# Performance work log

Hardware: AMD Instinct MI355X
Metric: run time of the kernel (lower is better)

## Reference

```python
import jax, jax.numpy as jnp
import numpy as np

# Grid config (LSS standard, matches init_kwargs)
XB = (-50.0, 50.0, 0.5)
YB = (-50.0, 50.0, 0.5)
ZB = (-10.0, 10.0, 20.0)
DB = (4.0, 45.0, 1.0)
FINAL_DIM = (256, 704)
DOWN = 16
CAMC = 64

DX = jnp.array([XB[2], YB[2], ZB[2]], jnp.float32)
BX = jnp.array([XB[0] + XB[2] / 2.0, YB[0] + YB[2] / 2.0, ZB[0] + ZB[2] / 2.0], jnp.float32)
NX0 = int((XB[1] - XB[0]) / XB[2])  # 200
NX1 = int((YB[1] - YB[0]) / YB[2])  # 200
NZ = int((ZB[1] - ZB[0]) / ZB[2])   # 1


def make_frustum():
    ogfH, ogfW = FINAL_DIM
    fH, fW = ogfH // DOWN, ogfW // DOWN
    ds = jnp.arange(DB[0], DB[1], DB[2], dtype=jnp.float32)  # [D]
    D = ds.shape[0]
    ds = jnp.broadcast_to(ds[:, None, None], (D, fH, fW))
    xs = jnp.broadcast_to(jnp.linspace(0.0, ogfW - 1, fW, dtype=jnp.float32)[None, None, :], (D, fH, fW))
    ys = jnp.broadcast_to(jnp.linspace(0.0, ogfH - 1, fH, dtype=jnp.float32)[None, :, None], (D, fH, fW))
    return jnp.stack((xs, ys, ds), -1)  # [D, fH, fW, 3]


def setup_inputs() -> dict:
    key = jax.random.key(0)
    B, N, D, fH, fW, C = 4, 6, 41, 16, 44, CAMC
    kx, kt = jax.random.split(key, 2)
    x = jax.random.normal(kx, (B, N, D, fH, fW, C), jnp.float32)
    # cam-to-ego base: cam z(forward)->ego x, cam x(right)->-ego y, cam y(down)->-ego z
    base = np.array([[0.0, 0.0, 1.0], [-1.0, 0.0, 0.0], [0.0, -1.0, 0.0]], np.float32)
    yaws = np.linspace(0.0, 2.0 * np.pi, N, endpoint=False).astype(np.float32)
    c, s = np.cos(yaws), np.sin(yaws)
    Rz = np.zeros((N, 3, 3), np.float32)
    Rz[:, 0, 0] = c; Rz[:, 0, 1] = -s; Rz[:, 1, 0] = s; Rz[:, 1, 1] = c; Rz[:, 2, 2] = 1.0
    rots_np = np.einsum('nij,jk->nik', Rz, base)
    rots = jnp.asarray(np.tile(rots_np[None], (B, 1, 1, 1)))
    # pinhole intrinsics for 704x256 image
    K = np.array([[550.0, 0.0, 352.0], [0.0, 550.0, 128.0], [0.0, 0.0, 1.0]], np.float32)
    intrins = jnp.asarray(np.tile(K[None, None], (B, N, 1, 1)))
    post_rots = jnp.asarray(np.tile(np.eye(3, dtype=np.float32)[None, None], (B, N, 1, 1)))
    post_trans = jnp.zeros((B, N, 3), jnp.float32)
    trans = jax.random.uniform(kt, (B, N, 3), jnp.float32, -1.5, 1.5)
    return {"x": x, "rots": rots, "trans": trans, "intrins": intrins,
            "post_rots": post_rots, "post_trans": post_trans}


def _forward(x, rots, trans, intrins, post_rots, post_trans):
    B, N, D, fH, fW, C = x.shape
    frustum = make_frustum()  # [D,fH,fW,3]

    # ---- get_geometry ----
    intrins_inv = jnp.linalg.inv(intrins)        # [B,N,3,3]
    post_rots_inv = jnp.linalg.inv(post_rots)    # [B,N,3,3]
    cam_to_ego = rots @ intrins_inv              # [B,N,3,3]
    pts = frustum[None, None] - post_trans[:, :, None, None, None, :]        # [B,N,D,fH,fW,3]
    # points @ post_rots_inv^T  ==  post_rots_inv @ points
    pts = jnp.einsum('bndhwc,bnkc->bndhwk', pts, post_rots_inv)
    pts = jnp.concatenate([pts[..., :2] * pts[..., 2:3], pts[..., 2:3]], -1)
    geom = jnp.einsum('bndhwc,bnkc->bndhwk', pts, cam_to_ego) + trans[:, :, None, None, None, :]

    # ---- voxel_pooling ----
    Nprime = B * N * D * fH * fW
    feats = x.reshape(Nprime, C)
    g = (geom - (BX - DX / 2.0)) / DX
    g = jnp.clip(g, -1e6, 1e6)
    g = jnp.trunc(g).astype(jnp.int32).reshape(Nprime, 3)  # torch .long() truncates toward zero
    batch_ix = jnp.repeat(jnp.arange(B, dtype=jnp.int32), Nprime // B)
    kept = ((g[:, 0] >= 0) & (g[:, 0] < NX0) &
            (g[:, 1] >= 0) & (g[:, 1] < NX1) &
            (g[:, 2] >= 0) & (g[:, 2] < NZ))
    # flat index into [B, NZ, NX0, NX1]; sort+cumsum_trick+scatter == segment-sum per voxel
    idx = batch_ix * (NZ * NX0 * NX1) + g[:, 2] * (NX0 * NX1) + g[:, 0] * NX1 + g[:, 1]
    idx = jnp.where(kept, idx, 0)
    w = kept.astype(feats.dtype)[:, None]
    pooled = jax.ops.segment_sum(feats * w, idx, num_segments=B * NZ * NX0 * NX1)
    final = pooled.reshape(B, NZ, NX0, NX1, C)
    # torch.cat(final.unbind(dim=2), 1) on [B,C,NZ,X,Y] -> [B, NZ*C, X, Y] (z-major)
    final = jnp.transpose(final, (0, 1, 4, 2, 3)).reshape(B, NZ * C, NX0, NX1)
    return final


def reference(x, rots, trans, intrins, post_rots, post_trans):
    return _forward(x, rots, trans, intrins, post_rots, post_trans)
```

## Files before the change

kernel.cpp:

```cpp
#include <hip/hip_runtime.h>
#include <cstddef>

#define NB   4
#define NN_  6
#define ND_  41
#define NFH  16
#define NFW  44
#define NC   64
#define NX0_ 200
#define NX1_ 200
#define NXY  (NX0_ * NX1_)
#define NCOL (NB * NN_ * ND_ * NFW)
#define NCELL (NB * NXY)
#define CAP   48
#define QMAX  (64 * CAP)

__device__ __forceinline__ void inv3(const float* a, float* inv) {
    float c00 = __fsub_rn(__fmul_rn(a[4], a[8]), __fmul_rn(a[5], a[7]));
    float c01 = __fsub_rn(__fmul_rn(a[5], a[6]), __fmul_rn(a[3], a[8]));
    float c02 = __fsub_rn(__fmul_rn(a[3], a[7]), __fmul_rn(a[4], a[6]));
    float det = __fadd_rn(__fadd_rn(__fmul_rn(a[0], c00), __fmul_rn(a[1], c01)),
                          __fmul_rn(a[2], c02));
    inv[0] = __fdiv_rn(c00, det);
    inv[1] = __fdiv_rn(__fsub_rn(__fmul_rn(a[2], a[7]), __fmul_rn(a[1], a[8])), det);
    inv[2] = __fdiv_rn(__fsub_rn(__fmul_rn(a[1], a[5]), __fmul_rn(a[2], a[4])), det);
    inv[3] = __fdiv_rn(c01, det);
    inv[4] = __fdiv_rn(__fsub_rn(__fmul_rn(a[0], a[8]), __fmul_rn(a[2], a[6])), det);
    inv[5] = __fdiv_rn(__fsub_rn(__fmul_rn(a[2], a[3]), __fmul_rn(a[0], a[5])), det);
    inv[6] = __fdiv_rn(c02, det);
    inv[7] = __fdiv_rn(__fsub_rn(__fmul_rn(a[1], a[6]), __fmul_rn(a[0], a[7])), det);
    inv[8] = __fdiv_rn(__fsub_rn(__fmul_rn(a[0], a[4]), __fmul_rn(a[1], a[3])), det);
}

__global__ void setup_kernel(const float* __restrict__ rots,
                             const float* __restrict__ trans,
                             const float* __restrict__ intrins,
                             const float* __restrict__ post_rots,
                             const float* __restrict__ post_trans,
                             float* __restrict__ mats) {
    int t = threadIdx.x;
    if (t >= NB * NN_) return;
    const float* R  = rots      + t * 9;
    const float* K  = intrins   + t * 9;
    const float* PR = post_rots + t * 9;
    float Kinv[9], Pinv[9];
    inv3(K, Kinv);
    inv3(PR, Pinv);
    float* o = mats + t * 24;
    for (int i = 0; i < 3; ++i)
        for (int k = 0; k < 3; ++k) {
            float s = __fmul_rn(R[i * 3 + 0], Kinv[0 * 3 + k]);
            s = __fadd_rn(s, __fmul_rn(R[i * 3 + 1], Kinv[1 * 3 + k]));
            s = __fadd_rn(s, __fmul_rn(R[i * 3 + 2], Kinv[2 * 3 + k]));
            o[i * 3 + k] = s;
        }
    for (int i = 0; i < 9; ++i) o[9 + i] = Pinv[i];
    o[18] = trans[t * 3 + 0];
    o[19] = trans[t * 3 + 1];
    o[20] = trans[t * 3 + 2];
    o[21] = post_trans[t * 3 + 0];
    o[22] = post_trans[t * 3 + 1];
    o[23] = post_trans[t * 3 + 2];
}

__device__ __forceinline__ void hw_fadd(float* p, float v) {
    asm volatile("global_atomic_add_f32 %0, %1, off" : : "v"(p), "v"(v) : "memory");
}

__device__ __forceinline__ int compute_idx(int b, int n, int d, int h, int w,
                                           const float* __restrict__ mats) {
    const float* mp = mats + (b * NN_ + n) * 24;

    float u   = (w == NFW - 1) ? 703.0f : (float)((double)w * (703.0 / 43.0));
    float v   = __fmul_rn((float)h, 17.0f);
    float dep = (float)(4 + d);

    float f0 = __fsub_rn(u, mp[21]);
    float f1 = __fsub_rn(v, mp[22]);
    float f2 = __fsub_rn(dep, mp[23]);

    float q0 = __fadd_rn(__fadd_rn(__fmul_rn(mp[9],  f0), __fmul_rn(mp[10], f1)), __fmul_rn(mp[11], f2));
    float q1 = __fadd_rn(__fadd_rn(__fmul_rn(mp[12], f0), __fmul_rn(mp[13], f1)), __fmul_rn(mp[14], f2));
    float q2 = __fadd_rn(__fadd_rn(__fmul_rn(mp[15], f0), __fmul_rn(mp[16], f1)), __fmul_rn(mp[17], f2));

    float r0 = __fmul_rn(q0, q2);
    float r1 = __fmul_rn(q1, q2);

    float g0 = __fadd_rn(__fadd_rn(__fadd_rn(__fmul_rn(mp[0], r0), __fmul_rn(mp[1], r1)), __fmul_rn(mp[2], q2)), mp[18]);
    float g1 = __fadd_rn(__fadd_rn(__fadd_rn(__fmul_rn(mp[3], r0), __fmul_rn(mp[4], r1)), __fmul_rn(mp[5], q2)), mp[19]);
    float g2 = __fadd_rn(__fadd_rn(__fadd_rn(__fmul_rn(mp[6], r0), __fmul_rn(mp[7], r1)), __fmul_rn(mp[8], q2)), mp[20]);

    float s0 = __fdiv_rn(__fsub_rn(g0, -50.0f), 0.5f);
    float s1 = __fdiv_rn(__fsub_rn(g1, -50.0f), 0.5f);
    float s2 = __fdiv_rn(__fsub_rn(g2, -10.0f), 20.0f);
    s0 = fminf(fmaxf(s0, -1e6f), 1e6f);
    s1 = fminf(fmaxf(s1, -1e6f), 1e6f);
    s2 = fminf(fmaxf(s2, -1e6f), 1e6f);
    int i0 = (int)s0;
    int i1 = (int)s1;
    int i2 = (int)s2;
    if (i0 >= 0 && i0 < NX0_ && i1 >= 0 && i1 < NX1_ && i2 >= 0 && i2 < 1)
        return b * NXY + i0 * NX1_ + i1;
    return -1;
}

__global__ __launch_bounds__(256) void build_lists(const float* __restrict__ mats,
                                                   int* __restrict__ cnt,
                                                   unsigned* __restrict__ lists) {
    int cid = blockIdx.x * 256 + threadIdx.x;
    if (cid >= NCOL) return;
    int w = cid % NFW; int t = cid / NFW;
    int d = t % ND_;   t /= ND_;
    int n = t % NN_;   int b = t / NN_;

    int first = -1;
    unsigned vm = 0, sm = 0;
    #pragma unroll
    for (int h = 0; h < 16; ++h) {
        int ih = compute_idx(b, n, d, h, w, mats);
        bool val = (ih >= 0);
        vm |= (val ? 1u : 0u) << h;
        if (first < 0 && val) first = ih;
        sm |= ((val && ih == first) ? 1u : 0u) << h;
    }
    if (vm == 0) return;
    if (sm == vm) {
        int slot = atomicAdd(&cnt[first], 1);
        if (slot < CAP) lists[(size_t)first * CAP + slot] = (vm << 16) | (unsigned)(cid & 0xffff);
    } else {
        #pragma unroll
        for (int h = 0; h < 16; ++h) {
            int ih = compute_idx(b, n, d, h, w, mats);
            if (ih >= 0) {
                int slot = atomicAdd(&cnt[ih], 1);
                if (slot < CAP) lists[(size_t)ih * CAP + slot] = (1u << (16 + h)) | (unsigned)(cid & 0xffff);
            }
        }
    }
}

__global__ __launch_bounds__(256) void gather_bev(const float* __restrict__ x,
                                                  const int* __restrict__ cnt,
                                                  const unsigned* __restrict__ lists,
                                                  float* __restrict__ out) {
    __shared__ float4 tile[64 * 16];
    __shared__ unsigned short items[QMAX];
    __shared__ int qcount;

    int b   = blockIdx.y;
    int xy0 = blockIdx.x * 64;

    if (threadIdx.x == 0) qcount = 0;
    #pragma unroll
    for (int s = 0; s < 4; ++s)
        tile[s * 256 + threadIdx.x] = make_float4(0.f, 0.f, 0.f, 0.f);
    __syncthreads();

    if (threadIdx.x < 64) {
        int ci = threadIdx.x;
        int c  = cnt[b * NXY + xy0 + ci];
        c = c < CAP ? c : CAP;
        if (c > 0) {
            int base = atomicAdd(&qcount, c);
            for (int e = 0; e < c; ++e)
                items[base + e] = (unsigned short)((ci << 8) | e);
        }
    }
    __syncthreads();
    int total = qcount;

    int g = threadIdx.x >> 4;
    int l = threadIdx.x & 15;
    const int HS = NFW * (NC / 4);

    for (int i = g; i < total; i += 16) {
        unsigned it = items[i];
        int ci = it >> 8, e = it & 255;
        unsigned ent = lists[(size_t)(b * NXY + xy0 + ci) * CAP + e];
        int cid = ent & 0xffff;
        unsigned hmask = ent >> 16;
        int w = cid % NFW; int t2 = cid / NFW;
        int d = t2 % ND_;  t2 /= ND_;
        int n = t2 % NN_;
        const float4* xp = (const float4*)
            (x + (((size_t)((b * NN_ + n) * ND_ + d) * NFH) * NFW + w) * NC) + l;

        float4 a = make_float4(0.f, 0.f, 0.f, 0.f);
        float4 v[8];
        #pragma unroll
        for (int j = 0; j < 8; ++j) v[j] = xp[j * HS];
        #pragma unroll
        for (int j = 0; j < 8; ++j) {
            float m = ((hmask >> j) & 1) ? 1.0f : 0.0f;
            a.x += v[j].x * m; a.y += v[j].y * m;
            a.z += v[j].z * m; a.w += v[j].w * m;
        }
        #pragma unroll
        for (int j = 0; j < 8; ++j) v[j] = xp[(8 + j) * HS];
        #pragma unroll
        for (int j = 0; j < 8; ++j) {
            float m = ((hmask >> (8 + j)) & 1) ? 1.0f : 0.0f;
            a.x += v[j].x * m; a.y += v[j].y * m;
            a.z += v[j].z * m; a.w += v[j].w * m;
        }

        float* tp = (float*)&tile[ci * 16 + (l ^ ((ci >> 2) & 15))];
        atomicAdd(tp + 0, a.x);
        atomicAdd(tp + 1, a.y);
        atomicAdd(tp + 2, a.z);
        atomicAdd(tp + 3, a.w);
    }
    __syncthreads();

    int lane = threadIdx.x & 63, wv = threadIdx.x >> 6;
    int q = lane & 15, lh = lane >> 4, i0 = q << 2;
    #pragma unroll
    for (int s = 0; s < 4; ++s) {
        int c  = s * 16 + wv * 4 + lh;
        int c4 = c >> 2, cr = c & 3;
        float4 vv;
        vv.x = ((const float*)&tile[(i0 + 0) * 16 + (c4 ^ q)])[cr];
        vv.y = ((const float*)&tile[(i0 + 1) * 16 + (c4 ^ q)])[cr];
        vv.z = ((const float*)&tile[(i0 + 2) * 16 + (c4 ^ q)])[cr];
        vv.w = ((const float*)&tile[(i0 + 3) * 16 + (c4 ^ q)])[cr];
        *(float4*)(out + ((size_t)(b * NC + c)) * NXY + xy0 + i0) = vv;
    }
}

__global__ __launch_bounds__(256) void col_pool_direct(const float* __restrict__ x,
                                                       const float* __restrict__ mats,
                                                       float* __restrict__ dst) {
    int cid = blockIdx.x * 8 + (threadIdx.x >> 5);
    int sub = threadIdx.x & 31;
    int l   = sub & 15;
    int hh  = sub >> 4;
    int w = cid % NFW; int t = cid / NFW;
    int d = t % ND_;   t /= ND_;
    int n = t % NN_;   int b = t / NN_;

    int myidx = compute_idx(b, n, d, l, w, mats);
    int idx8[8];
    #pragma unroll
    for (int j = 0; j < 8; ++j) idx8[j] = __shfl(myidx, hh * 8 + j, 32);

    int vmax = myidx;
    #pragma unroll
    for (int k = 1; k < 16; k <<= 1) vmax = max(vmax, __shfl_xor(vmax, k, 16));
    if (vmax < 0) return;

    const float4* xp = (const float4*)
        (x + (((size_t)((b * NN_ + n) * ND_ + d) * NFH) * NFW + w) * NC) + l;
    const int HSTRIDE = NFW * (NC / 4);
    #pragma unroll
    for (int j = 0; j < 8; ++j) {
        if (idx8[j] >= 0) {
            float4 v = xp[(hh * 8 + j) * HSTRIDE];
            int bb = idx8[j] / NXY, xy = idx8[j] % NXY;
            float* o = dst + ((size_t)(bb * NC + l * 4)) * NXY + xy;
            hw_fadd(o,           v.x);
            hw_fadd(o + NXY,     v.y);
            hw_fadd(o + 2 * NXY, v.z);
            hw_fadd(o + 3 * NXY, v.w);
        }
    }
}

extern "C" void kernel_launch(void* const* d_in, const int* in_sizes, int n_in,
                              void* d_out, int out_size, void* d_ws, size_t ws_size,
                              hipStream_t stream) {
    (void)in_sizes; (void)n_in; (void)out_size;
    const float* x          = (const float*)d_in[0];
    const float* rots       = (const float*)d_in[1];
    const float* trans      = (const float*)d_in[2];
    const float* intrins    = (const float*)d_in[3];
    const float* post_rots  = (const float*)d_in[4];
    const float* post_trans = (const float*)d_in[5];
    float* out = (float*)d_out;

    const size_t need = ((size_t)NCELL * (CAP + 1) + 1024) * sizeof(int);

    if (ws_size >= need) {
        int*      cnt   = (int*)d_ws;
        unsigned* lists = (unsigned*)(cnt + NCELL);
        float*    mats  = (float*)(lists + (size_t)NCELL * CAP);
        setup_kernel<<<1, 32, 0, stream>>>(rots, trans, intrins, post_rots, post_trans, mats);
        hipMemsetAsync(cnt, 0, (size_t)NCELL * sizeof(int), stream);
        build_lists<<<(NCOL + 255) / 256, 256, 0, stream>>>(mats, cnt, lists);
        gather_bev<<<dim3(NXY / 64, NB), 256, 0, stream>>>(x, cnt, lists, out);
    } else {
        float* mats = (float*)d_ws;
        setup_kernel<<<1, 32, 0, stream>>>(rots, trans, intrins, post_rots, post_trans, mats);
        hipMemsetAsync(out, 0, (size_t)NB * NC * NXY * sizeof(float), stream);
        col_pool_direct<<<NCOL / 8, 256, 0, stream>>>(x, mats, out);
    }
}
```

Measured before the change: 293.0 us.

## Precompute per-column feature sums while building voxel lists, gather sums in BEV pass

The list-building kernel now uses 16 threads per column. Each thread computes one height's voxel index, and shuffle reductions find the column's valid mask and whether all valid heights land in the same voxel. The same kernel streams x once in order and writes a masked per-column channel sum to a workspace buffer. The gather kernel then reads a single precomputed 256-byte sum when the list entry covers the full column, instead of 16 strided float4 loads per entry. It falls back to per-height loads only for split columns. The trade is an extra write and read of the colsum buffer and a larger workspace requirement, in exchange for streaming x sequentially rather than through scattered gather loads.

```diff
diff --git a/kernel.cpp b/kernel.cpp
--- a/kernel.cpp
+++ b/kernel.cpp
@@ -104,44 +104,91 @@
     return -1;
 }
 
-__global__ __launch_bounds__(256) void build_lists(const float* __restrict__ mats,
-                                                   int* __restrict__ cnt,
-                                                   unsigned* __restrict__ lists) {
-    int cid = blockIdx.x * 256 + threadIdx.x;
-    if (cid >= NCOL) return;
+__global__ __launch_bounds__(256) void colsum_build(const float* __restrict__ x,
+                                                    const float* __restrict__ mats,
+                                                    int* __restrict__ cnt,
+                                                    unsigned* __restrict__ lists,
+                                                    unsigned* __restrict__ aux,
+                                                    float4* __restrict__ colsum) {
+    int cid = blockIdx.x * 16 + (threadIdx.x >> 4);
+    int l   = threadIdx.x & 15;
     int w = cid % NFW; int t = cid / NFW;
     int d = t % ND_;   t /= ND_;
     int n = t % NN_;   int b = t / NN_;
 
-    int first = -1;
-    unsigned vm = 0, sm = 0;
-    #pragma unroll
-    for (int h = 0; h < 16; ++h) {
-        int ih = compute_idx(b, n, d, h, w, mats);
-        bool val = (ih >= 0);
-        vm |= (val ? 1u : 0u) << h;
-        if (first < 0 && val) first = ih;
-        sm |= ((val && ih == first) ? 1u : 0u) << h;
-    }
-    if (vm == 0) return;
-    if (sm == vm) {
-        int slot = atomicAdd(&cnt[first], 1);
-        if (slot < CAP) lists[(size_t)first * CAP + slot] = (vm << 16) | (unsigned)(cid & 0xffff);
+    int myidx = compute_idx(b, n, d, l, w, mats);
+
+    int vm   = (myidx >= 0) ? (1 << l) : 0;
+    int vmin = (myidx >= 0) ? myidx : 0x7fffffff;
+    int vmax = myidx;
+    #pragma unroll
+    for (int k = 1; k < 16; k <<= 1) {
+        vm  |= __shfl_xor(vm,  k, 16);
+        vmin = min(vmin, __shfl_xor(vmin, k, 16));
+        vmax = max(vmax, __shfl_xor(vmax, k, 16));
+    }
+    if (vmax < 0) return;
+    bool allsame = (vmin == vmax);
+
+    if (allsame) {
+        if (l == 0) {
+            int slot = atomicAdd(&cnt[vmax], 1);
+            if (slot < CAP)
+                lists[(size_t)vmax * CAP + slot] = ((unsigned)vm << 16) | (unsigned)cid;
+        }
     } else {
-        #pragma unroll
-        for (int h = 0; h < 16; ++h) {
-            int ih = compute_idx(b, n, d, h, w, mats);
-            if (ih >= 0) {
-                int slot = atomicAdd(&cnt[ih], 1);
-                if (slot < CAP) lists[(size_t)ih * CAP + slot] = (1u << (16 + h)) | (unsigned)(cid & 0xffff);
-            }
-        }
-    }
+        if (myidx >= 0) {
+            int slot = atomicAdd(&cnt[myidx], 1);
+            if (slot < CAP)
+                lists[(size_t)myidx * CAP + slot] = (1u << (16 + l)) | (unsigned)cid;
+        }
+    }
+    if (l == 0) aux[cid] = (unsigned)vm;
+
+    const float4* xp = (const float4*)
+        (x + (((size_t)((b * NN_ + n) * ND_ + d) * NFH) * NFW + w) * NC) + l;
+    const int HS = NFW * (NC / 4);
+
+    float4 v[8];
+    float4 A0 = make_float4(0.f, 0.f, 0.f, 0.f);
+    float4 A1 = make_float4(0.f, 0.f, 0.f, 0.f);
+    #pragma unroll
+    for (int j = 0; j < 8; ++j) v[j] = xp[j * HS];
+    #pragma unroll
+    for (int j = 0; j < 8; j += 2) {
+        float m0 = ((vm >> j) & 1) ? 1.0f : 0.0f;
+        float m1 = ((vm >> (j + 1)) & 1) ? 1.0f : 0.0f;
+        A0.x += v[j].x * m0;     A0.y += v[j].y * m0;
+        A0.z += v[j].z * m0;     A0.w += v[j].w * m0;
+        A1.x += v[j + 1].x * m1; A1.y += v[j + 1].y * m1;
+        A1.z += v[j + 1].z * m1; A1.w += v[j + 1].w * m1;
+    }
+    float4 s0 = make_float4(A0.x + A1.x, A0.y + A1.y, A0.z + A1.z, A0.w + A1.w);
+
+    float4 B0 = make_float4(0.f, 0.f, 0.f, 0.f);
+    float4 B1 = make_float4(0.f, 0.f, 0.f, 0.f);
+    #pragma unroll
+    for (int j = 0; j < 8; ++j) v[j] = xp[(8 + j) * HS];
+    #pragma unroll
+    for (int j = 0; j < 8; j += 2) {
+        float m0 = ((vm >> (8 + j)) & 1) ? 1.0f : 0.0f;
+        float m1 = ((vm >> (9 + j)) & 1) ? 1.0f : 0.0f;
+        B0.x += v[j].x * m0;     B0.y += v[j].y * m0;
+        B0.z += v[j].z * m0;     B0.w += v[j].w * m0;
+        B1.x += v[j + 1].x * m1; B1.y += v[j + 1].y * m1;
+        B1.z += v[j + 1].z * m1; B1.w += v[j + 1].w * m1;
+    }
+    float4 s1 = make_float4(B0.x + B1.x, B0.y + B1.y, B0.z + B1.z, B0.w + B1.w);
+
+    colsum[(size_t)cid * 16 + l] =
+        make_float4(s0.x + s1.x, s0.y + s1.y, s0.z + s1.z, s0.w + s1.w);
 }
 
 __global__ __launch_bounds__(256) void gather_bev(const float* __restrict__ x,
                                                   const int* __restrict__ cnt,
                                                   const unsigned* __restrict__ lists,
+                                                  const unsigned* __restrict__ aux,
+                                                  const float4* __restrict__ colsum,
                                                   float* __restrict__ out) {
     __shared__ float4 tile[64 * 16];
     __shared__ unsigned short items[QMAX];
@@ -179,29 +226,24 @@
         unsigned ent = lists[(size_t)(b * NXY + xy0 + ci) * CAP + e];
         int cid = ent & 0xffff;
         unsigned hmask = ent >> 16;
-        int w = cid % NFW; int t2 = cid / NFW;
-        int d = t2 % ND_;  t2 /= ND_;
-        int n = t2 % NN_;
-        const float4* xp = (const float4*)
-            (x + (((size_t)((b * NN_ + n) * ND_ + d) * NFH) * NFW + w) * NC) + l;
-
-        float4 a = make_float4(0.f, 0.f, 0.f, 0.f);
-        float4 v[8];
-        #pragma unroll
-        for (int j = 0; j < 8; ++j) v[j] = xp[j * HS];
-        #pragma unroll
-        for (int j = 0; j < 8; ++j) {
-            float m = ((hmask >> j) & 1) ? 1.0f : 0.0f;
-            a.x += v[j].x * m; a.y += v[j].y * m;
-            a.z += v[j].z * m; a.w += v[j].w * m;
-        }
-        #pragma unroll
-        for (int j = 0; j < 8; ++j) v[j] = xp[(8 + j) * HS];
-        #pragma unroll
-        for (int j = 0; j < 8; ++j) {
-            float m = ((hmask >> (8 + j)) & 1) ? 1.0f : 0.0f;
-            a.x += v[j].x * m; a.y += v[j].y * m;
-            a.z += v[j].z * m; a.w += v[j].w * m;
+
+        float4 a;
+        if (__builtin_expect(hmask == aux[cid], 1)) {
+            a = colsum[(size_t)cid * 16 + l];
+        } else {
+            int w = cid % NFW; int t2 = cid / NFW;
+            int d = t2 % ND_;  t2 /= ND_;
+            int n = t2 % NN_;
+            const float4* xp = (const float4*)
+                (x + (((size_t)((b * NN_ + n) * ND_ + d) * NFH) * NFW + w) * NC) + l;
+            a = make_float4(0.f, 0.f, 0.f, 0.f);
+            #pragma unroll
+            for (int j = 0; j < 16; ++j) {
+                if ((hmask >> j) & 1) {
+                    float4 vv = xp[j * HS];
+                    a.x += vv.x; a.y += vv.y; a.z += vv.z; a.w += vv.w;
+                }
+            }
         }
 
         float* tp = (float*)&tile[ci * 16 + (l ^ ((ci >> 2) & 15))];
@@ -277,16 +319,19 @@
     const float* post_trans = (const float*)d_in[5];
     float* out = (float*)d_out;
 
-    const size_t need = ((size_t)NCELL * (CAP + 1) + 1024) * sizeof(int);
+    const size_t colsum_f = (size_t)NCOL * NC;
+    const size_t need = (colsum_f + NCELL * (size_t)(CAP + 1) + NCOL + 1024) * 4;
 
     if (ws_size >= need) {
-        int*      cnt   = (int*)d_ws;
-        unsigned* lists = (unsigned*)(cnt + NCELL);
-        float*    mats  = (float*)(lists + (size_t)NCELL * CAP);
+        float4*   colsum = (float4*)d_ws;
+        int*      cnt    = (int*)((float*)d_ws + colsum_f);
+        unsigned* lists  = (unsigned*)(cnt + NCELL);
+        unsigned* aux    = lists + (size_t)NCELL * CAP;
+        float*    mats   = (float*)(aux + NCOL);
         setup_kernel<<<1, 32, 0, stream>>>(rots, trans, intrins, post_rots, post_trans, mats);
         hipMemsetAsync(cnt, 0, (size_t)NCELL * sizeof(int), stream);
-        build_lists<<<(NCOL + 255) / 256, 256, 0, stream>>>(mats, cnt, lists);
-        gather_bev<<<dim3(NXY / 64, NB), 256, 0, stream>>>(x, cnt, lists, out);
+        colsum_build<<<NCOL / 16, 256, 0, stream>>>(x, mats, cnt, lists, aux, colsum);
+        gather_bev<<<dim3(NXY / 64, NB), 256, 0, stream>>>(x, cnt, lists, aux, colsum, out);
     } else {
         float* mats = (float*)d_ws;
         setup_kernel<<<1, 32, 0, stream>>>(rots, trans, intrins, post_rots, post_trans, mats);
```

Result: slower. 305.7 us (+4.3%).
